# Optimization experiments

Hardware: AMD Instinct MI355X
Metric: run time of the kernel (lower is better)

Reference implementation:

```python
import jax, jax.numpy as jnp
import numpy as np

BANDWIDTH = 50.0
EPS = 1e-8


def setup_inputs() -> dict:
    key = jax.random.key(0)
    k1, k2, k3 = jax.random.split(key, 3)
    B, n, N_full = 4096, 8, 16384
    z = jax.random.normal(k1, (B, n), dtype=jnp.float32)
    # Precomputed RBF kernel stand-in: values in (0,1], like exp(-dist_sq/bw)
    K_full = jax.random.uniform(k2, (N_full, N_full), dtype=jnp.float32)
    indices = jax.random.randint(k3, (B,), 0, N_full)
    return {"z": z, "K_full": K_full, "indices": indices}


def _laplacian_from_kernel(K, bandwidth):
    # D_inv @ K @ D_inv is just row/col scaling by 1/d
    c = 0.25
    d = K.sum(axis=1) + EPS                      # (B,)
    K_tilde = K / (d[:, None] * d[None, :])      # (B,B)
    d_tilde = K_tilde.sum(axis=1) + EPS          # (B,)
    N = K.shape[0]
    L = (K_tilde / d_tilde[:, None] - jnp.eye(N, dtype=K.dtype)) / (c * bandwidth)
    return L


def _compute_JGinvJT(L, z):
    N, n = z.shape
    outer = z[:, :, None] * z[:, None, :]                    # (N,n,n)
    term1 = (L @ outer.reshape(N, n * n)).reshape(N, n, n)   # L @ (z_i z_j)
    LY = L @ z                                               # (N,n)
    term2 = z[:, :, None] * LY[:, None, :]
    term3 = LY[:, :, None] * z[:, None, :]
    return 0.5 * (term1 - term2 - term3)


def _relaxed_distortion(H):
    n = H.shape[-1]
    TrH = jnp.trace(H, axis1=-2, axis2=-1)                   # (N,)
    TrH2 = jnp.einsum('nij,nji->n', H, H)                    # Tr(H@H) without materializing H@H
    return (TrH2 - 2.0 * TrH + n).mean()


def reference(z, K_full, indices):
    K_batch = K_full[indices][:, indices]                    # (B,B) double gather
    L = _laplacian_from_kernel(K_batch, BANDWIDTH)
    H = _compute_JGinvJT(L, z)
    return _relaxed_distortion(H)
```

## Files before the change

kernel.cpp:

```cpp
#include <hip/hip_runtime.h>

#define EPSF 1e-8f
#define BN 4096
#define NF 16384
#define SCALE 12.5f
#define SINV 0.08f

template <bool STORE>
__global__ __launch_bounds__(256) void k_gather_d(
    const float* __restrict__ Kf, const int* __restrict__ idx,
    float* __restrict__ Kb, float* __restrict__ dv, float* __restrict__ wv) {
  const int i = blockIdx.x;
  const int t = threadIdx.x;
  const size_t base = (size_t)idx[i] * (size_t)NF;
  float s = 0.f;
#pragma unroll
  for (int jt = 0; jt < 16; ++jt) {
    const int j = jt * 256 + t;
    const float v = Kf[base + (size_t)idx[j]];
    if (STORE) Kb[(size_t)i * BN + j] = v;
    s += v;
  }
#pragma unroll
  for (int o = 32; o > 0; o >>= 1) s += __shfl_down(s, o, 64);
  __shared__ float red[4];
  if ((t & 63) == 0) red[t >> 6] = s;
  __syncthreads();
  if (t == 0) {
    const float tot = red[0] + red[1] + red[2] + red[3] + EPSF;
    dv[i] = tot;
    wv[i] = 1.0f / tot;
  }
}

template <bool GATHER>
__global__ __launch_bounds__(256) void k_rows(
    const float* __restrict__ Ksrc, const int* __restrict__ idx,
    const float* __restrict__ z, const float* __restrict__ dv,
    const float* __restrict__ wv, float* __restrict__ lossv) {
  const int i = blockIdx.x;
  const int t = threadIdx.x;
  const size_t base = GATHER ? (size_t)idx[i] * (size_t)NF : (size_t)i * BN;

  float vals[45];
#pragma unroll
  for (int k = 0; k < 45; ++k) vals[k] = 0.f;

  const float4* z4 = (const float4*)z;
  for (int jt = 0; jt < 16; ++jt) {
    const int j = jt * 256 + t;
    const float kv = GATHER ? Ksrc[base + (size_t)idx[j]] : Ksrc[base + j];
    const float kw = kv * wv[j];
    const float4 za = z4[2 * j];
    const float4 zb = z4[2 * j + 1];
    float zz[8] = {za.x, za.y, za.z, za.w, zb.x, zb.y, zb.z, zb.w};
    float q[8];
#pragma unroll
    for (int a = 0; a < 8; ++a) {
      q[a] = kw * zz[a];
      vals[36 + a] += q[a];
    }
    vals[44] += kw;
    int k = 0;
#pragma unroll
    for (int a = 0; a < 8; ++a)
#pragma unroll
      for (int b = a; b < 8; ++b) {
        vals[k] += q[a] * zz[b];
        ++k;
      }
  }

#pragma unroll
  for (int k = 0; k < 45; ++k) {
    float v = vals[k];
#pragma unroll
    for (int o = 32; o > 0; o >>= 1) v += __shfl_down(v, o, 64);
    vals[k] = v;
  }
  __shared__ float red[4][45];
  if ((t & 63) == 0) {
#pragma unroll
    for (int k = 0; k < 45; ++k) red[t >> 6][k] = vals[k];
  }
  __syncthreads();

  if (t == 0) {
    float S[36], U[8], T0;
#pragma unroll
    for (int k = 0; k < 36; ++k) S[k] = red[0][k] + red[1][k] + red[2][k] + red[3][k];
#pragma unroll
    for (int a = 0; a < 8; ++a)
      U[a] = red[0][36 + a] + red[1][36 + a] + red[2][36 + a] + red[3][36 + a];
    T0 = red[0][44] + red[1][44] + red[2][44] + red[3][44];

    const float di = dv[i];
    const float wi = wv[i];
    const float dt = T0 * wi + EPSF;
    const float alpha = 1.0f / (di * dt * SCALE);

    const float4 za = z4[2 * i];
    const float4 zb = z4[2 * i + 1];
    float zi[8] = {za.x, za.y, za.z, za.w, zb.x, zb.y, zb.z, zb.w};
    float u[8];
#pragma unroll
    for (int a = 0; a < 8; ++a) u[a] = alpha * U[a];

    float trH = 0.f, tr2 = 0.f;
    int k = 0;
#pragma unroll
    for (int a = 0; a < 8; ++a)
#pragma unroll
      for (int b = a; b < 8; ++b) {
        const float H =
            0.5f * (alpha * S[k] + SINV * zi[a] * zi[b] - zi[a] * u[b] - u[a] * zi[b]);
        if (a == b) {
          trH += H;
          tr2 += H * H;
        } else {
          tr2 += 2.f * H * H;
        }
        ++k;
      }
    lossv[i] = tr2 - 2.f * trH;
  }
}

__global__ __launch_bounds__(256) void k_final(const float* __restrict__ lossv,
                                               float* __restrict__ out) {
  const int t = threadIdx.x;
  float s = 0.f;
  for (int i = t; i < BN; i += 256) s += lossv[i];
#pragma unroll
  for (int o = 32; o > 0; o >>= 1) s += __shfl_down(s, o, 64);
  __shared__ float red[4];
  if ((t & 63) == 0) red[t >> 6] = s;
  __syncthreads();
  if (t == 0) out[0] = (red[0] + red[1] + red[2] + red[3]) / (float)BN + 8.0f;
}

extern "C" void kernel_launch(void* const* d_in, const int* in_sizes, int n_in,
                              void* d_out, int out_size, void* d_ws, size_t ws_size,
                              hipStream_t stream) {
  const float* z = (const float*)d_in[0];
  const float* Kf = (const float*)d_in[1];
  const int* idx = (const int*)d_in[2];
  float* out = (float*)d_out;

  char* ws = (char*)d_ws;
  const size_t kb_bytes = (size_t)BN * BN * sizeof(float);
  const bool store = ws_size >= kb_bytes + 3 * BN * sizeof(float);

  float *Kb, *dv, *wv, *lossv;
  if (store) {
    Kb = (float*)ws;
    dv = (float*)(ws + kb_bytes);
  } else {
    Kb = nullptr;
    dv = (float*)ws;
  }
  wv = dv + BN;
  lossv = wv + BN;

  if (store) {
    k_gather_d<true><<<BN, 256, 0, stream>>>(Kf, idx, Kb, dv, wv);
    k_rows<false><<<BN, 256, 0, stream>>>(Kb, idx, z, dv, wv, lossv);
  } else {
    k_gather_d<false><<<BN, 256, 0, stream>>>(Kf, idx, nullptr, dv, wv);
    k_rows<true><<<BN, 256, 0, stream>>>(Kf, idx, z, dv, wv, lossv);
  }
  k_final<<<1, 256, 0, stream>>>(lossv, out);
}
```

Measured before the change: 1.286 ms.

## Sort gather indices and permute z to improve gather locality

Adds a single-block bitonic sort of the index array, carrying along a permutation that is applied to z. The gather kernels then use the sorted indices, so the column reads within each row of K_full hit addresses in increasing order, which should give better cache-line and DRAM-page reuse. The loss is invariant to a consistent permutation of the batch, so the result is unchanged. This costs one extra single-workgroup kernel launch and more workspace, and the sort runs serially on one CU.

```diff
diff --git a/kernel.cpp b/kernel.cpp
--- a/kernel.cpp
+++ b/kernel.cpp
@@ -5,6 +5,47 @@
 #define NF 16384
 #define SCALE 12.5f
 #define SINV 0.08f
+
+__global__ __launch_bounds__(1024) void k_sort(const int* __restrict__ idx,
+                                               const float* __restrict__ z,
+                                               int* __restrict__ sidx,
+                                               float* __restrict__ z_perm) {
+  __shared__ int key[BN];
+  __shared__ int pos[BN];
+  const int t = threadIdx.x;
+  for (int e = t; e < BN; e += 1024) {
+    key[e] = idx[e];
+    pos[e] = e;
+  }
+  for (int k = 2; k <= BN; k <<= 1) {
+    for (int jj = k >> 1; jj > 0; jj >>= 1) {
+      __syncthreads();
+      for (int ii = t; ii < BN; ii += 1024) {
+        const int p = ii ^ jj;
+        if (p > ii) {
+          const int a = key[ii], b = key[p];
+          const bool up = ((ii & k) == 0);
+          if ((a > b) == up) {
+            key[ii] = b;
+            key[p] = a;
+            const int tp = pos[ii];
+            pos[ii] = pos[p];
+            pos[p] = tp;
+          }
+        }
+      }
+    }
+  }
+  __syncthreads();
+  const float4* z4 = (const float4*)z;
+  float4* zp4 = (float4*)z_perm;
+  for (int e = t; e < BN; e += 1024) {
+    sidx[e] = key[e];
+    const int src = pos[e];
+    zp4[2 * e] = z4[2 * src];
+    zp4[2 * e + 1] = z4[2 * src + 1];
+  }
+}
 
 template <bool STORE>
 __global__ __launch_bounds__(256) void k_gather_d(
@@ -149,25 +190,28 @@
 
   char* ws = (char*)d_ws;
   const size_t kb_bytes = (size_t)BN * BN * sizeof(float);
-  const bool store = ws_size >= kb_bytes + 3 * BN * sizeof(float);
-
-  float *Kb, *dv, *wv, *lossv;
+  const size_t aux_bytes =
+      (3 * BN + BN) * sizeof(float) + BN * sizeof(int) + BN * 8 * sizeof(float);
+  const bool store = ws_size >= kb_bytes + aux_bytes;
+
   if (store) {
-    Kb = (float*)ws;
-    dv = (float*)(ws + kb_bytes);
+    float* Kb = (float*)ws;
+    float* dv = (float*)(ws + kb_bytes);
+    float* wv = dv + BN;
+    float* lossv = wv + BN;
+    int* sidx = (int*)(lossv + BN);
+    float* z_perm = (float*)(sidx + BN);
+
+    k_sort<<<1, 1024, 0, stream>>>(idx, z, sidx, z_perm);
+    k_gather_d<true><<<BN, 256, 0, stream>>>(Kf, sidx, Kb, dv, wv);
+    k_rows<false><<<BN, 256, 0, stream>>>(Kb, sidx, z_perm, dv, wv, lossv);
+    k_final<<<1, 256, 0, stream>>>(lossv, out);
   } else {
-    Kb = nullptr;
-    dv = (float*)ws;
-  }
-  wv = dv + BN;
-  lossv = wv + BN;
-
-  if (store) {
-    k_gather_d<true><<<BN, 256, 0, stream>>>(Kf, idx, Kb, dv, wv);
-    k_rows<false><<<BN, 256, 0, stream>>>(Kb, idx, z, dv, wv, lossv);
-  } else {
+    float* dv = (float*)ws;
+    float* wv = dv + BN;
+    float* lossv = wv + BN;
     k_gather_d<false><<<BN, 256, 0, stream>>>(Kf, idx, nullptr, dv, wv);
     k_rows<true><<<BN, 256, 0, stream>>>(Kf, idx, z, dv, wv, lossv);
-  }
-  k_final<<<1, 256, 0, stream>>>(lossv, out);
-}
+    k_final<<<1, 256, 0, stream>>>(lossv, out);
+  }
+}
```

Measured after the change: 1.320 ms. 1.03x slower.
